# Kernel tuning notes

Measured on AMD Instinct MI355X. Metric: run time of the kernel, lower is better.

## Reference

```python
import jax, jax.numpy as jnp
import numpy as np

B, S, D, H, C = 128, 2048, 128, 128, 10  # batch, seq_len, input_size, hidden_size, num_classes


def setup_inputs() -> dict:
    key = jax.random.key(0)
    ks = jax.random.split(key, 11)
    k = 1.0 / np.sqrt(H)  # PyTorch RNN init scale
    u = lambda kk, shp: jax.random.uniform(kk, shp, jnp.float32, -k, k)
    return {
        "x": jax.random.normal(ks[0], (B, S, D), jnp.float32),
        # layer 0 (input D -> hidden H); gate order: r, z, n (PyTorch convention)
        "W_ih0": u(ks[1], (3 * H, D)), "W_hh0": u(ks[2], (3 * H, H)),
        "b_ih0": u(ks[3], (3 * H,)),   "b_hh0": u(ks[4], (3 * H,)),
        # layer 1 (hidden H -> hidden H)
        "W_ih1": u(ks[5], (3 * H, H)), "W_hh1": u(ks[6], (3 * H, H)),
        "b_ih1": u(ks[7], (3 * H,)),   "b_hh1": u(ks[8], (3 * H,)),
        # output linear H -> C
        "W_out": u(ks[9], (C, H)), "b_out": u(ks[10], (C,)),
    }


def _gru_layer(x, W_ih, W_hh, b_ih, b_hh):
    """Single unidirectional GRU layer, PyTorch math. x: [B,S,Din] -> ([B,S,H], h_last [B,H])."""
    Bs = x.shape[0]
    Hh = W_hh.shape[1]
    # Precompute all input projections in one big GEMM: [S,B,3H]
    xp = jnp.einsum('bsd,gd->sbg', x, W_ih) + b_ih
    h0 = jnp.zeros((Bs, Hh), x.dtype)

    def step(h, xp_t):
        hp = h @ W_hh.T + b_hh                      # [B,3H]
        xr, xz, xn = jnp.split(xp_t, 3, axis=-1)
        hr, hz, hn = jnp.split(hp, 3, axis=-1)
        r = jax.nn.sigmoid(xr + hr)                 # reset gate
        z = jax.nn.sigmoid(xz + hz)                 # update gate
        n = jnp.tanh(xn + r * hn)                   # new gate
        h_new = (1.0 - z) * n + z * h
        return h_new, h_new

    h_last, hs = jax.lax.scan(step, h0, xp)         # hs: [S,B,H]
    return jnp.transpose(hs, (1, 0, 2)), h_last


def reference(x, W_ih0, W_hh0, b_ih0, b_hh0, W_ih1, W_hh1, b_ih1, b_hh1, W_out, b_out):
    y0, _ = _gru_layer(x, W_ih0, W_hh0, b_ih0, b_hh0)
    _, h_last = _gru_layer(y0, W_ih1, W_hh1, b_ih1, b_hh1)
    # dropout between layers is disabled at inference (eval mode)
    return h_last @ W_out.T + b_out                 # [B,C] logits
```

## Files before the change

### kernel.cpp

```cpp
#include <hip/hip_runtime.h>
#include <hip/hip_bf16.h>


using bf16x8 = __attribute__((ext_vector_type(8))) short;
using s16x4  = __attribute__((ext_vector_type(4))) short;
using f32x4  = __attribute__((ext_vector_type(4))) float;
using f16x8  = __attribute__((ext_vector_type(8))) _Float16;
using f16x4  = __attribute__((ext_vector_type(4))) _Float16;
using u32x2  = __attribute__((ext_vector_type(2))) unsigned int;

#define S_LEN 2048
#define D_IN  128
#define HID   128
#define B_TOT 128
#define BC    16
#define PAD   136
#define G3    384
#define M_TOT (B_TOT * S_LEN)

#define CH    32
#define WIN   4
#define TILE_HALFS (BC * HID)
#define WGWIN_HALFS (WIN * CH * TILE_HALFS)

#define OP    104

__device__ __forceinline__ float bf2f(short s) {
  unsigned int u = ((unsigned int)(unsigned short)s) << 16;
  float f; __builtin_memcpy(&f, &u, 4); return f;
}
__device__ __forceinline__ short f2bf(float f) {
  unsigned int u; __builtin_memcpy(&u, &f, 4);
  u += 0x7fffu + ((u >> 16) & 1u);
  return (short)(u >> 16);
}
__device__ __forceinline__ float fast_sigmoid(float x) {
  return __builtin_amdgcn_rcpf(1.f + __expf(-x));
}
__device__ __forceinline__ float fast_tanh(float x) {
  return 2.f * __builtin_amdgcn_rcpf(1.f + __expf(-2.f * x)) - 1.f;
}
__device__ __forceinline__ f32x4 MFMA(bf16x8 a, bf16x8 b, f32x4 c) {
  return __builtin_amdgcn_mfma_f32_16x16x32_bf16(a, b, c, 0, 0, 0);
}
__device__ __forceinline__ f32x4 MFMA16(f16x8 a, f16x8 b, f32x4 c) {
  return __builtin_amdgcn_mfma_f32_16x16x32_f16(a, b, c, 0, 0, 0);
}
__device__ __forceinline__ void loadA(bf16x8 (&a)[4], const short* p) {
#pragma unroll
  for (int kq = 0; kq < 4; ++kq) a[kq] = *(const bf16x8*)(p + kq * 32);
}
__device__ __forceinline__ void loadA16(f16x8 (&a)[4], const _Float16* p) {
#pragma unroll
  for (int kq = 0; kq < 4; ++kq) a[kq] = *(const f16x8*)(p + kq * 32);
}
__device__ __forceinline__ void wg_barrier() {
  asm volatile("s_waitcnt lgkmcnt(0)\n\ts_barrier" ::: "memory");
}
__device__ __forceinline__ int ld_acq(const int* p) {
  return __hip_atomic_load(p, __ATOMIC_ACQUIRE, __HIP_MEMORY_SCOPE_AGENT);
}
__device__ __forceinline__ int ld_rlx(const int* p) {
  return __hip_atomic_load(p, __ATOMIC_RELAXED, __HIP_MEMORY_SCOPE_AGENT);
}
__device__ __forceinline__ void st_rel(int* p, int v) {
  __hip_atomic_store(p, v, __ATOMIC_RELEASE, __HIP_MEMORY_SCOPE_AGENT);
}

__global__ __launch_bounds__(256, 1) void xp0_gemm(
    const float* __restrict__ x, const float* __restrict__ Wih0,
    const float* __restrict__ bih0, const float* __restrict__ bhh0,
    _Float16* __restrict__ xp0)
{
  __shared__ _Float16 wlds[96 * PAD];
  __shared__ float bfold[G3];

  const int tid = threadIdx.x;
  const int w = tid >> 6, lane = tid & 63, nw = lane & 15, quad = lane >> 4;
  const int m0 = blockIdx.x * 64 + w * 16;

  for (int g = tid; g < G3; g += 256)
    bfold[g] = bih0[g] + (g < 256 ? bhh0[g] : 0.f);

  f16x8 af[4];
  const int arow = m0 + nw;
#pragma unroll
  for (int kq = 0; kq < 4; ++kq) {
    const float* p = x + (size_t)arow * D_IN + kq * 32 + quad * 8;
    float4 v0 = *(const float4*)p, v1 = *(const float4*)(p + 4);
    af[kq] = (f16x8){(_Float16)v0.x, (_Float16)v0.y, (_Float16)v0.z, (_Float16)v0.w,
                     (_Float16)v1.x, (_Float16)v1.y, (_Float16)v1.z, (_Float16)v1.w};
  }

  for (int grp = 0; grp < 4; ++grp) {
    __syncthreads();
    for (int i = tid; i < 96 * 128 / 4; i += 256) {
      const int idx = i * 4, row = idx >> 7, cc = idx & 127;
      float4 v = *(const float4*)(Wih0 + (size_t)(grp * 96 + row) * 128 + cc);
      f16x4 s = { (_Float16)v.x, (_Float16)v.y, (_Float16)v.z, (_Float16)v.w };
      *(f16x4*)&wlds[row * PAD + cc] = s;
    }
    __syncthreads();

    f32x4 acc[6];
#pragma unroll
    for (int i = 0; i < 6; ++i) acc[i] = (f32x4){0.f, 0.f, 0.f, 0.f};
#pragma unroll
    for (int tI = 0; tI < 6; ++tI)
#pragma unroll
      for (int kq = 0; kq < 4; ++kq) {
        f16x8 b = *(const f16x8*)&wlds[(tI * 16 + nw) * PAD + kq * 32 + quad * 8];
        acc[tI] = MFMA16(af[kq], b, acc[tI]);
      }

    __syncthreads();
#pragma unroll
    for (int tI = 0; tI < 6; ++tI) {
      const float bb = bfold[grp * 96 + tI * 16 + nw];
#pragma unroll
      for (int rr = 0; rr < 4; ++rr)
        wlds[(w * 16 + quad * 4 + rr) * OP + tI * 16 + nw] =
            (_Float16)(acc[tI][rr] + bb);
    }
    __syncthreads();
    {
      const int row = tid >> 2, ch = tid & 3;
      const _Float16* src = &wlds[row * OP + ch * 24];
      _Float16* dst = xp0 + (size_t)(blockIdx.x * 64 + row) * G3 + grp * 96 + ch * 24;
      *(f16x8*)(dst)      = *(const f16x8*)(src);
      *(f16x8*)(dst + 8)  = *(const f16x8*)(src + 8);
      *(f16x8*)(dst + 16) = *(const f16x8*)(src + 16);
    }
  }
}

__device__ __forceinline__ void mm3f(const f16x8 (&a)[4], const f16x8 (&W)[3][4],
                                     f32x4& r, f32x4& z, f32x4& n) {
#pragma unroll
  for (int kq = 0; kq < 4; ++kq) {
    r = MFMA16(a[kq], W[0][kq], r);
    z = MFMA16(a[kq], W[1][kq], z);
    n = MFMA16(a[kq], W[2][kq], n);
  }
}
__device__ __forceinline__ void mm3x2f(const f16x8 (&a)[4],
    const f16x8 (&Wa)[3][4], const f16x8 (&Wb)[3][4],
    f32x4& r1, f32x4& z1, f32x4& n1, f32x4& r2, f32x4& z2, f32x4& n2) {
#pragma unroll
  for (int kq = 0; kq < 4; ++kq) {
    r1 = MFMA16(a[kq], Wa[0][kq], r1);
    r2 = MFMA16(a[kq], Wb[0][kq], r2);
    z1 = MFMA16(a[kq], Wa[1][kq], z1);
    z2 = MFMA16(a[kq], Wb[1][kq], z2);
    n1 = MFMA16(a[kq], Wa[2][kq], n1);
    n2 = MFMA16(a[kq], Wb[2][kq], n2);
  }
}

__global__ __launch_bounds__(512, 2) void gru2_split(
    const _Float16* __restrict__ xp0,
    _Float16* __restrict__ win,
    int* __restrict__ ctrl,
    const float* __restrict__ Whh0, const float* __restrict__ bhh0,
    const float* __restrict__ Wih1, const float* __restrict__ Whh1,
    const float* __restrict__ bih1, const float* __restrict__ bhh1,
    const float* __restrict__ Wout, const float* __restrict__ bout,
    float* __restrict__ out)
{
  __shared__ _Float16 hf[2][BC * PAD];

  const int bid  = blockIdx.x;
  const int role = bid >> 3;
  const int g    = bid & 7;
  const int tid  = threadIdx.x;
  const int w    = tid >> 6;
  const int lane = tid & 63;
  const int nw   = lane & 15;
  const int quad = lane >> 4;
  const int col  = w * 16 + nw;
  const int b0   = g * BC;
  const int aoff = nw * PAD + quad * 8;

  int* flagp = ctrl + g;
  int* consp = ctrl + 8 + g;
  _Float16* win_g = win + (size_t)g * WGWIN_HALFS;

  for (int i = tid; i < 2 * BC * PAD; i += 512)
    ((_Float16*)hf)[i] = (_Float16)0.f;

  if (role == 0) {
    const float b0n_h = bhh0[256 + col];
    f16x8 Wh0[3][4];
#pragma unroll
    for (int gg = 0; gg < 3; ++gg)
#pragma unroll
      for (int kq = 0; kq < 4; ++kq) {
        const size_t o = (size_t)(gg * 128 + col) * HID + kq * 32 + quad * 8;
#pragma unroll
        for (int e = 0; e < 8; ++e) Wh0[gg][kq][e] = (_Float16)Whh0[o + e];
      }

    size_t xbase[4];
#pragma unroll
    for (int rr = 0; rr < 4; ++rr)
      xbase[rr] = (size_t)(b0 + quad * 4 + rr) * S_LEN * G3 + col;

    auto loadPK = [&](float (&P)[12], int t) {
      const size_t tG = (size_t)t * G3;
#pragma unroll
      for (int gg = 0; gg < 3; ++gg)
#pragma unroll
        for (int rr = 0; rr < 4; ++rr)
          P[gg * 4 + rr] = (float)xp0[xbase[rr] + tG + gg * 128];
    };

    float PA[12], PB[12];
    loadPK(PA, 0);
    loadPK(PB, 1);

    f32x4 h0r = {0.f, 0.f, 0.f, 0.f};
    const int cpo = (tid >> 5) * PAD + ((4 * tid) & 127);
    int cons_seen = 0;
    __syncthreads();

    auto pstep = [&](float (&P)[12], const int t, const int pr, const int pw) {
      if ((t & (CH - 1)) == 0) {
        const int need = (t >> 5) - (WIN - 1);
        if (need > 0 && cons_seen < need) {
          do { cons_seen = ld_rlx(consp);
               if (cons_seen < need) __builtin_amdgcn_s_sleep(8);
          } while (cons_seen < need);
        }
      }

      f32x4 ar = {P[0], P[1], P[2], P[3]};
      f32x4 az = {P[4], P[5], P[6], P[7]};
      f32x4 ahn = {b0n_h, b0n_h, b0n_h, b0n_h};
      f16x8 a[4];
      loadA16(a, &hf[pr][aoff]);
      mm3f(a, Wh0, ar, az, ahn);
#pragma unroll
      for (int rr = 0; rr < 4; ++rr) {
        float r = fast_sigmoid(ar[rr]);
        float z = fast_sigmoid(az[rr]);
        float n = fast_tanh(P[8 + rr] + r * ahn[rr]);
        float h = n + z * (h0r[rr] - n);
        h0r[rr] = h;
        hf[pw][(quad * 4 + rr) * PAD + col] = (_Float16)h;
      }
      wg_barrier();
      {
        u32x2 v;
        __builtin_memcpy(&v, &hf[pw][cpo], 8);
        _Float16* dst = win_g +
            ((size_t)((t >> 5) & (WIN - 1)) * CH + (t & (CH - 1))) * TILE_HALFS
            + 4 * tid;
        __builtin_nontemporal_store(v, (u32x2*)dst);
      }
      if ((t & (CH - 1)) == (CH - 1)) {
        __syncthreads();
        if (tid == 0) st_rel(flagp, (t >> 5) + 1);
      }
      const int tn = (t + 2 < S_LEN) ? t + 2 : t;
      loadPK(P, tn);
    };

#pragma unroll 1
    for (int tt = 0; tt < S_LEN; tt += 2) {
      pstep(PA, tt,     0, 1);
      pstep(PB, tt + 1, 1, 0);
    }
  } else {
    const float b1r   = bih1[col]       + bhh1[col];
    const float b1z   = bih1[128 + col] + bhh1[128 + col];
    const float b1n_i = bih1[256 + col];
    const float b1n_h = bhh1[256 + col];

    f16x8 Wi1[3][4], Wh1[3][4];
#pragma unroll
    for (int gg = 0; gg < 3; ++gg)
#pragma unroll
      for (int kq = 0; kq < 4; ++kq) {
        const size_t o = (size_t)(gg * 128 + col) * HID + kq * 32 + quad * 8;
#pragma unroll
        for (int e = 0; e < 8; ++e) {
          Wi1[gg][kq][e] = (_Float16)Wih1[o + e];
          Wh1[gg][kq][e] = (_Float16)Whh1[o + e];
        }
      }

    const int afroff = nw * 128 + quad * 8;
    f32x4 h1r = {0.f, 0.f, 0.f, 0.f};
    int seen = 0;
    __syncthreads();

    while (seen < 1) { seen = ld_acq(flagp);
                       if (seen < 1) __builtin_amdgcn_s_sleep(8); }
    f16x8 Anext[4];
    f32x4 xp1r = {b1r, b1r, b1r, b1r};
    f32x4 xp1z = {b1z, b1z, b1z, b1z};
    f32x4 xp1n = {b1n_i, b1n_i, b1n_i, b1n_i};
    {
      f16x8 A0[4];
#pragma unroll
      for (int kq = 0; kq < 4; ++kq)
        A0[kq] = *(const f16x8*)(win_g + afroff + kq * 32);
      mm3f(A0, Wi1, xp1r, xp1z, xp1n);
    }
#pragma unroll
    for (int kq = 0; kq < 4; ++kq)
      Anext[kq] = *(const f16x8*)(win_g + TILE_HALFS + afroff + kq * 32);

    auto cstep = [&](const int t, const int pr, const int pw) {
      if ((t & (CH - 1)) == 0 && tid == 0) st_rel(consp, t >> 5);
      f16x8 hfr[4];
      loadA16(hfr, &hf[pr][aoff]);
      f32x4 br  = xp1r;
      f32x4 bz  = xp1z;
      f32x4 bxn = xp1n;
      f32x4 bhn = {b1n_h, b1n_h, b1n_h, b1n_h};
      mm3f(hfr, Wh1, br, bz, bhn);
#pragma unroll
      for (int rr = 0; rr < 4; ++rr) {
        float r = fast_sigmoid(br[rr]);
        float z = fast_sigmoid(bz[rr]);
        float n = fast_tanh(bxn[rr] + r * bhn[rr]);
        float h = n + z * (h1r[rr] - n);
        h1r[rr] = h;
        hf[pw][(quad * 4 + rr) * PAD + col] = (_Float16)h;
      }
      xp1r = (f32x4){b1r, b1r, b1r, b1r};
      xp1z = (f32x4){b1z, b1z, b1z, b1z};
      xp1n = (f32x4){b1n_i, b1n_i, b1n_i, b1n_i};
      mm3f(Anext, Wi1, xp1r, xp1z, xp1n);
      const int tp2 = (t + 2 < S_LEN) ? t + 2 : S_LEN - 1;
      const int cn2 = (tp2 >> 5) + 1;
      if (seen < cn2) {
        do { seen = ld_acq(flagp);
             if (seen < cn2) __builtin_amdgcn_s_sleep(8);
        } while (seen < cn2);
      }
      {
        const _Float16* tp = win_g +
            ((size_t)((tp2 >> 5) & (WIN - 1)) * CH + (tp2 & (CH - 1))) * TILE_HALFS
            + afroff;
#pragma unroll
        for (int kq = 0; kq < 4; ++kq) Anext[kq] = *(const f16x8*)(tp + kq * 32);
      }
      wg_barrier();
    };

#pragma unroll 1
    for (int tt = 0; tt < S_LEN; tt += 2) {
      cstep(tt,     0, 1);
      cstep(tt + 1, 1, 0);
    }

    if (tid < BC * 10) {
      const int b = tid / 10, c = tid % 10;
      float s = bout[c];
      const _Float16* hh = &hf[0][b * PAD];
#pragma unroll 8
      for (int k = 0; k < HID; ++k)
        s += (float)hh[k] * Wout[c * HID + k];
      out[(size_t)(b0 + b) * 10 + c] = s;
    }
  }
}

__global__ __launch_bounds__(512, 2) void gru2_rec(
    const _Float16* __restrict__ xp0,
    const float* __restrict__ Whh0, const float* __restrict__ bhh0,
    const float* __restrict__ Wih1, const float* __restrict__ Whh1,
    const float* __restrict__ bih1, const float* __restrict__ bhh1,
    const float* __restrict__ Wout, const float* __restrict__ bout,
    float* __restrict__ out)
{
  __shared__ _Float16 h0f[2][BC * PAD];
  __shared__ _Float16 h1f[2][BC * PAD];

  const int tid  = threadIdx.x;
  const int w    = tid >> 6;
  const int lane = tid & 63;
  const int nw   = lane & 15;
  const int quad = lane >> 4;
  const int col  = w * 16 + nw;
  const int b0   = blockIdx.x * BC;

  for (int i = tid; i < 2 * BC * PAD; i += 512) {
    ((_Float16*)h0f)[i] = (_Float16)0.f;
    ((_Float16*)h1f)[i] = (_Float16)0.f;
  }

  const float b0n_h = bhh0[256 + col];
  const float b1r   = bih1[col]       + bhh1[col];
  const float b1z   = bih1[128 + col] + bhh1[128 + col];
  const float b1n_i = bih1[256 + col];
  const float b1n_h = bhh1[256 + col];

  f16x8 Wh0[3][4], Wi1[3][4], Wh1[3][4];
#pragma unroll
  for (int g = 0; g < 3; ++g) {
#pragma unroll
    for (int kq = 0; kq < 4; ++kq) {
      const size_t o = (size_t)(g * 128 + col) * HID + kq * 32 + quad * 8;
#pragma unroll
      for (int e = 0; e < 8; ++e) {
        Wh0[g][kq][e] = (_Float16)Whh0[o + e];
        Wi1[g][kq][e] = (_Float16)Wih1[o + e];
        Wh1[g][kq][e] = (_Float16)Whh1[o + e];
      }
    }
  }

  size_t xbase[4];
#pragma unroll
  for (int rr = 0; rr < 4; ++rr)
    xbase[rr] = (size_t)(b0 + quad * 4 + rr) * S_LEN * G3 + col;

  float P[12];
#pragma unroll
  for (int g = 0; g < 3; ++g)
#pragma unroll
    for (int rr = 0; rr < 4; ++rr)
      P[g * 4 + rr] = (float)xp0[xbase[rr] + g * 128];

  f32x4 h0r = {0.f, 0.f, 0.f, 0.f}, h1r = {0.f, 0.f, 0.f, 0.f};
  wg_barrier();

  const int aoff = nw * PAD + quad * 8;

  for (int t = 0; t < S_LEN; ++t) {
    const int pr = t & 1, pw = pr ^ 1;
    const int tn = (t + 1 < S_LEN) ? t + 1 : t;
    float Pn[12];
#pragma unroll
    for (int g = 0; g < 3; ++g)
#pragma unroll
      for (int rr = 0; rr < 4; ++rr)
        Pn[g * 4 + rr] = (float)xp0[xbase[rr] + (size_t)tn * G3 + g * 128];

    f32x4 ar  = {P[0], P[1], P[2], P[3]};
    f32x4 az  = {P[4], P[5], P[6], P[7]};
    f32x4 ahn = {b0n_h, b0n_h, b0n_h, b0n_h};
    f32x4 br  = {b1r, b1r, b1r, b1r};
    f32x4 bz  = {b1z, b1z, b1z, b1z};
    f32x4 bxn = {b1n_i, b1n_i, b1n_i, b1n_i};
    f32x4 bhn = {b1n_h, b1n_h, b1n_h, b1n_h};

    f16x8 a[4];
    loadA16(a, &h0f[pr][aoff]); mm3x2f(a, Wh0, Wi1, ar, az, ahn, br, bz, bxn);
    loadA16(a, &h1f[pr][aoff]); mm3f(a, Wh1, br, bz, bhn);

#pragma unroll
    for (int rr = 0; rr < 4; ++rr) {
      float r = fast_sigmoid(ar[rr]);
      float z = fast_sigmoid(az[rr]);
      float n = fast_tanh(P[8 + rr] + r * ahn[rr]);
      float h = n + z * (h0r[rr] - n);
      h0r[rr] = h;
      h0f[pw][(quad * 4 + rr) * PAD + col] = (_Float16)h;
    }
    if (t) {
#pragma unroll
      for (int rr = 0; rr < 4; ++rr) {
        float r = fast_sigmoid(br[rr]);
        float z = fast_sigmoid(bz[rr]);
        float n = fast_tanh(bxn[rr] + r * bhn[rr]);
        float h = n + z * (h1r[rr] - n);
        h1r[rr] = h;
        h1f[pw][(quad * 4 + rr) * PAD + col] = (_Float16)h;
      }
    }
#pragma unroll
    for (int i = 0; i < 12; ++i) P[i] = Pn[i];
    wg_barrier();
  }

  {
    f32x4 br  = {b1r, b1r, b1r, b1r};
    f32x4 bz  = {b1z, b1z, b1z, b1z};
    f32x4 bxn = {b1n_i, b1n_i, b1n_i, b1n_i};
    f32x4 bhn = {b1n_h, b1n_h, b1n_h, b1n_h};
    f16x8 a[4];
    loadA16(a, &h0f[0][aoff]); mm3f(a, Wi1, br, bz, bxn);
    loadA16(a, &h1f[0][aoff]); mm3f(a, Wh1, br, bz, bhn);
#pragma unroll
    for (int rr = 0; rr < 4; ++rr) {
      float r = fast_sigmoid(br[rr]);
      float z = fast_sigmoid(bz[rr]);
      float n = fast_tanh(bxn[rr] + r * bhn[rr]);
      float h = n + z * (h1r[rr] - n);
      h1f[1][(quad * 4 + rr) * PAD + col] = (_Float16)h;
    }
    wg_barrier();
  }

  if (tid < BC * 10) {
    const int b = tid / 10, c = tid % 10;
    float s = bout[c];
    const _Float16* hh = &h1f[1][b * PAD];
#pragma unroll 8
    for (int k = 0; k < HID; ++k)
      s += (float)hh[k] * Wout[c * HID + k];
    out[(size_t)(b0 + b) * 10 + c] = s;
  }
}

template<bool NSEP>
__device__ __forceinline__ void mm6(const bf16x8 (&a)[4], const bf16x8 (&W)[6][4],
                                    f32x4 (&acc)[6], f32x4 (&accn)[2]) {
#pragma unroll
  for (int tI = 0; tI < 6; ++tI)
#pragma unroll
    for (int kq = 0; kq < 4; ++kq) {
      if (NSEP && tI >= 4) accn[tI - 4] = MFMA(a[kq], W[tI][kq], accn[tI - 4]);
      else                 acc[tI]      = MFMA(a[kq], W[tI][kq], acc[tI]);
    }
}

__global__ __launch_bounds__(256, 1) void gru2_v1(
    const float* __restrict__ x,
    const float* __restrict__ Wih0, const float* __restrict__ Whh0,
    const float* __restrict__ bih0, const float* __restrict__ bhh0,
    const float* __restrict__ Wih1, const float* __restrict__ Whh1,
    const float* __restrict__ bih1, const float* __restrict__ bhh1,
    const float* __restrict__ Wout, const float* __restrict__ bout,
    float* __restrict__ out)
{
  __shared__ short h0hi[2][BC * PAD], h0lo[2][BC * PAD];
  __shared__ short h1hi[2][BC * PAD], h1lo[2][BC * PAD];
  __shared__ short xbhi[2][BC * PAD], xblo[2][BC * PAD];

  const int tid = threadIdx.x, w = tid >> 6, lane = tid & 63;
  const int nw = lane & 15, quad = lane >> 4, u0 = w * 32;
  const int b0 = blockIdx.x * BC;

  for (int i = tid; i < BC * PAD; i += 256) {
    h0hi[0][i] = 0; h0lo[0][i] = 0; h1hi[0][i] = 0; h1lo[0][i] = 0;
  }
  const size_t xelem = (size_t)(b0 + (tid >> 4)) * (size_t)(S_LEN * D_IN) + (size_t)((tid & 15) * 8);
  const int xsoff = (tid >> 4) * PAD + (tid & 15) * 8;

  auto load_x = [&](int t, bf16x8& xhi, bf16x8& xlo) {
    const size_t o = xelem + (size_t)t * D_IN;
    float4 v0 = *(const float4*)(x + o), v1 = *(const float4*)(x + o + 4);
    float v[8] = {v0.x, v0.y, v0.z, v0.w, v1.x, v1.y, v1.z, v1.w};
#pragma unroll
    for (int e = 0; e < 8; ++e) {
      short h = f2bf(v[e]); xhi[e] = h; xlo[e] = f2bf(v[e] - bf2f(h));
    }
  };
  { bf16x8 xh, xl; load_x(0, xh, xl);
    *(bf16x8*)&xbhi[0][xsoff] = xh; *(bf16x8*)&xblo[0][xsoff] = xl; }

  float brz0[4], bn0[4], brz1[4], bn1[4];
#pragma unroll
  for (int i = 0; i < 2; ++i) {
    const int c = u0 + i * 16 + nw;
    brz0[i] = bih0[c] + bhh0[c];     brz0[2 + i] = bih0[128 + c] + bhh0[128 + c];
    bn0[i] = bih0[256 + c];          bn0[2 + i] = bhh0[256 + c];
    brz1[i] = bih1[c] + bhh1[c];     brz1[2 + i] = bih1[128 + c] + bhh1[128 + c];
    bn1[i] = bih1[256 + c];          bn1[2 + i] = bhh1[256 + c];
  }

  bf16x8 W0[6][4], Wh0f[6][4], W1[6][4], Wh1f[6][4];
#pragma unroll
  for (int tI = 0; tI < 6; ++tI) {
    const int rb = (tI >> 1) * 128 + u0 + (tI & 1) * 16 + nw;
#pragma unroll
    for (int kq = 0; kq < 4; ++kq) {
      const size_t o = (size_t)rb * HID + kq * 32 + quad * 8;
#pragma unroll
      for (int e = 0; e < 8; ++e) {
        W0[tI][kq][e] = f2bf(Wih0[o + e]);  Wh0f[tI][kq][e] = f2bf(Whh0[o + e]);
        W1[tI][kq][e] = f2bf(Wih1[o + e]);  Wh1f[tI][kq][e] = f2bf(Whh1[o + e]);
      }
    }
  }

  f32x4 h0reg[2] = {{0,0,0,0},{0,0,0,0}}, h1reg[2] = {{0,0,0,0},{0,0,0,0}};
  const f32x4 ZV = {0.f, 0.f, 0.f, 0.f};
  __syncthreads();
  const int aoff = nw * PAD + quad * 8;

  auto gates = [&](const f32x4 (&acc)[6], const f32x4 (&accn)[2], f32x4 (&hreg)[2],
                   const float (&brz)[4], const float (&bn)[4],
                   short* dhi, short* dlo) {
#pragma unroll
    for (int i = 0; i < 2; ++i) {
      const int c = u0 + i * 16 + nw;
#pragma unroll
      for (int rr = 0; rr < 4; ++rr) {
        float rv = fast_sigmoid(acc[i][rr] + brz[i]);
        float zv = fast_sigmoid(acc[2 + i][rr] + brz[2 + i]);
        float nv = fast_tanh((acc[4 + i][rr] + bn[i]) + rv * (accn[i][rr] + bn[2 + i]));
        float h = (1.f - zv) * nv + zv * hreg[i][rr];
        hreg[i][rr] = h;
        short hi = f2bf(h);
        const int row = quad * 4 + rr;
        dhi[row * PAD + c] = hi;
        dlo[row * PAD + c] = f2bf(h - bf2f(hi));
      }
    }
  };

  for (int t = 0; t < S_LEN; ++t) {
    const int pr = t & 1, pw = pr ^ 1;
    const int t1 = (t + 1 < S_LEN) ? t + 1 : t;
    bf16x8 xh, xl; load_x(t1, xh, xl);

    f32x4 acc[6], accn[2];
#pragma unroll
    for (int i = 0; i < 6; ++i) acc[i] = ZV;
#pragma unroll
    for (int i = 0; i < 2; ++i) accn[i] = ZV;
    bf16x8 a[4];
    loadA(a, &xbhi[pr][aoff]); mm6<false>(a, W0, acc, accn);
    loadA(a, &xblo[pr][aoff]); mm6<false>(a, W0, acc, accn);
    loadA(a, &h0hi[pr][aoff]); mm6<true >(a, Wh0f, acc, accn);
    loadA(a, &h0lo[pr][aoff]); mm6<true >(a, Wh0f, acc, accn);
    gates(acc, accn, h0reg, brz0, bn0, h0hi[pw], h0lo[pw]);
    __syncthreads();

#pragma unroll
    for (int i = 0; i < 6; ++i) acc[i] = ZV;
#pragma unroll
    for (int i = 0; i < 2; ++i) accn[i] = ZV;
    loadA(a, &h0hi[pw][aoff]); mm6<false>(a, W1, acc, accn);
    loadA(a, &h0lo[pw][aoff]); mm6<false>(a, W1, acc, accn);
    loadA(a, &h1hi[pr][aoff]); mm6<true >(a, Wh1f, acc, accn);
    loadA(a, &h1lo[pr][aoff]); mm6<true >(a, Wh1f, acc, accn);
    *(bf16x8*)&xbhi[pw][xsoff] = xh;
    *(bf16x8*)&xblo[pw][xsoff] = xl;
    gates(acc, accn, h1reg, brz1, bn1, h1hi[pw], h1lo[pw]);
    __syncthreads();
  }

  if (tid < BC * 10) {
    const int b = tid / 10, c = tid % 10;
    float s = bout[c];
    const short* hh = &h1hi[0][b * PAD];
    const short* hl = &h1lo[0][b * PAD];
#pragma unroll 8
    for (int k = 0; k < HID; ++k)
      s += (bf2f(hh[k]) + bf2f(hl[k])) * Wout[c * HID + k];
    out[(size_t)(b0 + b) * 10 + c] = s;
  }
}

extern "C" void kernel_launch(void* const* d_in, const int* in_sizes, int n_in,
                              void* d_out, int out_size, void* d_ws, size_t ws_size,
                              hipStream_t stream) {
  (void)in_sizes; (void)n_in; (void)out_size;
  const float* x    = (const float*)d_in[0];
  const float* Wih0 = (const float*)d_in[1];
  const float* Whh0 = (const float*)d_in[2];
  const float* bih0 = (const float*)d_in[3];
  const float* bhh0 = (const float*)d_in[4];
  const float* Wih1 = (const float*)d_in[5];
  const float* Whh1 = (const float*)d_in[6];
  const float* bih1 = (const float*)d_in[7];
  const float* bhh1 = (const float*)d_in[8];
  const float* Wout = (const float*)d_in[9];
  const float* bout = (const float*)d_in[10];
  float* out = (float*)d_out;

  const size_t XPB  = (size_t)M_TOT * G3 * sizeof(_Float16);
  const size_t WINB = 8ull * WGWIN_HALFS * sizeof(_Float16);
  const size_t REQ  = XPB + WINB + 64;

  if (ws_size >= REQ) {
    char* ws = (char*)d_ws;
    _Float16* xp0  = (_Float16*)ws;
    _Float16* wing = (_Float16*)(ws + XPB);
    int*      ctrl = (int*)(ws + XPB + WINB);
    (void)hipMemsetAsync(ctrl, 0, 64, stream);
    xp0_gemm<<<dim3(M_TOT / 64), dim3(256), 0, stream>>>(
        x, Wih0, bih0, bhh0, xp0);
    gru2_split<<<dim3(16), dim3(512), 0, stream>>>(
        xp0, wing, ctrl, Whh0, bhh0, Wih1, Whh1, bih1, bhh1, Wout, bout, out);
  } else if (ws_size >= XPB) {
    xp0_gemm<<<dim3(M_TOT / 64), dim3(256), 0, stream>>>(
        x, Wih0, bih0, bhh0, (_Float16*)d_ws);
    gru2_rec<<<dim3(B_TOT / BC), dim3(512), 0, stream>>>(
        (const _Float16*)d_ws, Whh0, bhh0, Wih1, Whh1, bih1, bhh1, Wout, bout, out);
  } else {
    gru2_v1<<<dim3(B_TOT / BC), dim3(256), 0, stream>>>(
        x, Wih0, Whh0, bih0, bhh0, Wih1, Whh1, bih1, bhh1, Wout, bout, out);
  }
}
```

Before: 2.305 ms.

## Fuse input-projection GEMM into recurrent kernel with per-chunk readiness flags

```diff
diff --git a/kernel.cpp b/kernel.cpp
--- a/kernel.cpp
+++ b/kernel.cpp
@@ -24,6 +24,8 @@
 #define WGWIN_HALFS (WIN * CH * TILE_HALFS)
 
 #define OP    104
+#define P1B   2048
+#define TCH   128
 
 __device__ __forceinline__ float bf2f(short s) {
   unsigned int u = ((unsigned int)(unsigned short)s) << 16;
@@ -67,116 +69,101 @@
   __hip_atomic_store(p, v, __ATOMIC_RELEASE, __HIP_MEMORY_SCOPE_AGENT);
 }
 
-__global__ __launch_bounds__(256, 1) void xp0_gemm(
+__global__ __launch_bounds__(512, 2) void gru2_all(
     const float* __restrict__ x, const float* __restrict__ Wih0,
     const float* __restrict__ bih0, const float* __restrict__ bhh0,
-    _Float16* __restrict__ xp0)
-{
-  __shared__ _Float16 wlds[96 * PAD];
-  __shared__ float bfold[G3];
-
-  const int tid = threadIdx.x;
-  const int w = tid >> 6, lane = tid & 63, nw = lane & 15, quad = lane >> 4;
-  const int m0 = blockIdx.x * 64 + w * 16;
-
-  for (int g = tid; g < G3; g += 256)
-    bfold[g] = bih0[g] + (g < 256 ? bhh0[g] : 0.f);
-
-  f16x8 af[4];
-  const int arow = m0 + nw;
-#pragma unroll
-  for (int kq = 0; kq < 4; ++kq) {
-    const float* p = x + (size_t)arow * D_IN + kq * 32 + quad * 8;
-    float4 v0 = *(const float4*)p, v1 = *(const float4*)(p + 4);
-    af[kq] = (f16x8){(_Float16)v0.x, (_Float16)v0.y, (_Float16)v0.z, (_Float16)v0.w,
-                     (_Float16)v1.x, (_Float16)v1.y, (_Float16)v1.z, (_Float16)v1.w};
-  }
-
-  for (int grp = 0; grp < 4; ++grp) {
-    __syncthreads();
-    for (int i = tid; i < 96 * 128 / 4; i += 256) {
-      const int idx = i * 4, row = idx >> 7, cc = idx & 127;
-      float4 v = *(const float4*)(Wih0 + (size_t)(grp * 96 + row) * 128 + cc);
-      f16x4 s = { (_Float16)v.x, (_Float16)v.y, (_Float16)v.z, (_Float16)v.w };
-      *(f16x4*)&wlds[row * PAD + cc] = s;
-    }
-    __syncthreads();
-
-    f32x4 acc[6];
-#pragma unroll
-    for (int i = 0; i < 6; ++i) acc[i] = (f32x4){0.f, 0.f, 0.f, 0.f};
-#pragma unroll
-    for (int tI = 0; tI < 6; ++tI)
-#pragma unroll
-      for (int kq = 0; kq < 4; ++kq) {
-        f16x8 b = *(const f16x8*)&wlds[(tI * 16 + nw) * PAD + kq * 32 + quad * 8];
-        acc[tI] = MFMA16(af[kq], b, acc[tI]);
-      }
-
-    __syncthreads();
-#pragma unroll
-    for (int tI = 0; tI < 6; ++tI) {
-      const float bb = bfold[grp * 96 + tI * 16 + nw];
-#pragma unroll
-      for (int rr = 0; rr < 4; ++rr)
-        wlds[(w * 16 + quad * 4 + rr) * OP + tI * 16 + nw] =
-            (_Float16)(acc[tI][rr] + bb);
-    }
-    __syncthreads();
-    {
-      const int row = tid >> 2, ch = tid & 3;
-      const _Float16* src = &wlds[row * OP + ch * 24];
-      _Float16* dst = xp0 + (size_t)(blockIdx.x * 64 + row) * G3 + grp * 96 + ch * 24;
-      *(f16x8*)(dst)      = *(const f16x8*)(src);
-      *(f16x8*)(dst + 8)  = *(const f16x8*)(src + 8);
-      *(f16x8*)(dst + 16) = *(const f16x8*)(src + 16);
-    }
-  }
-}
-
-__device__ __forceinline__ void mm3f(const f16x8 (&a)[4], const f16x8 (&W)[3][4],
-                                     f32x4& r, f32x4& z, f32x4& n) {
-#pragma unroll
-  for (int kq = 0; kq < 4; ++kq) {
-    r = MFMA16(a[kq], W[0][kq], r);
-    z = MFMA16(a[kq], W[1][kq], z);
-    n = MFMA16(a[kq], W[2][kq], n);
-  }
-}
-__device__ __forceinline__ void mm3x2f(const f16x8 (&a)[4],
-    const f16x8 (&Wa)[3][4], const f16x8 (&Wb)[3][4],
-    f32x4& r1, f32x4& z1, f32x4& n1, f32x4& r2, f32x4& z2, f32x4& n2) {
-#pragma unroll
-  for (int kq = 0; kq < 4; ++kq) {
-    r1 = MFMA16(a[kq], Wa[0][kq], r1);
-    r2 = MFMA16(a[kq], Wb[0][kq], r2);
-    z1 = MFMA16(a[kq], Wa[1][kq], z1);
-    z2 = MFMA16(a[kq], Wb[1][kq], z2);
-    n1 = MFMA16(a[kq], Wa[2][kq], n1);
-    n2 = MFMA16(a[kq], Wb[2][kq], n2);
-  }
-}
-
-__global__ __launch_bounds__(512, 2) void gru2_split(
-    const _Float16* __restrict__ xp0,
-    _Float16* __restrict__ win,
-    int* __restrict__ ctrl,
-    const float* __restrict__ Whh0, const float* __restrict__ bhh0,
+    _Float16* __restrict__ xp0,
+    _Float16* __restrict__ win, int* __restrict__ ctrl,
+    const float* __restrict__ Whh0, const float* __restrict__ bhh0b,
     const float* __restrict__ Wih1, const float* __restrict__ Whh1,
     const float* __restrict__ bih1, const float* __restrict__ bhh1,
     const float* __restrict__ Wout, const float* __restrict__ bout,
     float* __restrict__ out)
 {
-  __shared__ _Float16 hf[2][BC * PAD];
+  __shared__ __align__(16) char smem[28160];
 
   const int bid  = blockIdx.x;
-  const int role = bid >> 3;
-  const int g    = bid & 7;
   const int tid  = threadIdx.x;
   const int w    = tid >> 6;
   const int lane = tid & 63;
   const int nw   = lane & 15;
   const int quad = lane >> 4;
+
+  if (bid >= 16) {
+    _Float16* wlds = (_Float16*)smem;
+    float* bfold = (float*)(smem + 26624);
+
+    const int p  = bid - 16;
+    const int b  = p & 127;
+    const int tc = p >> 7;
+    const int mb = b * S_LEN + tc * TCH;
+    const int m0 = mb + w * 16;
+
+    for (int g = tid; g < G3; g += 512)
+      bfold[g] = bih0[g] + (g < 256 ? bhh0[g] : 0.f);
+
+    f16x8 af[4];
+    const int arow = m0 + nw;
+#pragma unroll
+    for (int kq = 0; kq < 4; ++kq) {
+      const float* px = x + (size_t)arow * D_IN + kq * 32 + quad * 8;
+      float4 v0 = *(const float4*)px, v1 = *(const float4*)(px + 4);
+      af[kq] = (f16x8){(_Float16)v0.x, (_Float16)v0.y, (_Float16)v0.z, (_Float16)v0.w,
+                       (_Float16)v1.x, (_Float16)v1.y, (_Float16)v1.z, (_Float16)v1.w};
+    }
+
+    for (int grp = 0; grp < 4; ++grp) {
+      __syncthreads();
+      for (int i = tid; i < 96 * 128 / 4; i += 512) {
+        const int idx = i * 4, row = idx >> 7, cc = idx & 127;
+        float4 v = *(const float4*)(Wih0 + (size_t)(grp * 96 + row) * 128 + cc);
+        f16x4 s = { (_Float16)v.x, (_Float16)v.y, (_Float16)v.z, (_Float16)v.w };
+        *(f16x4*)&wlds[row * PAD + cc] = s;
+      }
+      __syncthreads();
+
+      f32x4 acc[6];
+#pragma unroll
+      for (int i = 0; i < 6; ++i) acc[i] = (f32x4){0.f, 0.f, 0.f, 0.f};
+#pragma unroll
+      for (int tI = 0; tI < 6; ++tI)
+#pragma unroll
+        for (int kq = 0; kq < 4; ++kq) {
+          f16x8 bfr = *(const f16x8*)&wlds[(tI * 16 + nw) * PAD + kq * 32 + quad * 8];
+          acc[tI] = MFMA16(af[kq], bfr, acc[tI]);
+        }
+
+      __syncthreads();
+#pragma unroll
+      for (int tI = 0; tI < 6; ++tI) {
+        const float bb = bfold[grp * 96 + tI * 16 + nw];
+#pragma unroll
+        for (int rr = 0; rr < 4; ++rr)
+          wlds[(w * 16 + quad * 4 + rr) * OP + tI * 16 + nw] =
+              (_Float16)(acc[tI][rr] + bb);
+      }
+      __syncthreads();
+      {
+        const int row = tid >> 2, ch = tid & 3;
+        const _Float16* src = &wlds[row * OP + ch * 24];
+        _Float16* dst = xp0 + (size_t)(mb + row) * G3 + grp * 96 + ch * 24;
+        *(f16x8*)(dst)      = *(const f16x8*)(src);
+        *(f16x8*)(dst + 8)  = *(const f16x8*)(src + 8);
+        *(f16x8*)(dst + 16) = *(const f16x8*)(src + 16);
+      }
+    }
+    __syncthreads();
+    if (tid == 0)
+      (void)__hip_atomic_fetch_add(ctrl + 16 + tc, 1, __ATOMIC_RELEASE,
+                                   __HIP_MEMORY_SCOPE_AGENT);
+    return;
+  }
+
+  _Float16 (&hf)[2][BC * PAD] =
+      *reinterpret_cast<_Float16 (*)[2][BC * PAD]>(smem);
+
+  const int role = bid >> 3;
+  const int g    = bid & 7;
   const int col  = w * 16 + nw;
   const int b0   = g * BC;
   const int aoff = nw * PAD + quad * 8;
@@ -189,7 +176,7 @@
     ((_Float16*)hf)[i] = (_Float16)0.f;
 
   if (role == 0) {
-    const float b0n_h = bhh0[256 + col];
+    const float b0n_h = bhh0b[256 + col];
     f16x8 Wh0[3][4];
 #pragma unroll
     for (int gg = 0; gg < 3; ++gg)
@@ -204,6 +191,13 @@
 #pragma unroll
     for (int rr = 0; rr < 4; ++rr)
       xbase[rr] = (size_t)(b0 + quad * 4 + rr) * S_LEN * G3 + col;
+
+    int chunk_seen = 0;
+    auto wait_chunk = [&](int c) {
+      if (chunk_seen > c) return;
+      while (ld_acq(ctrl + 16 + c) < 128) __builtin_amdgcn_s_sleep(8);
+      chunk_seen = c + 1;
+    };
 
     auto loadPK = [&](float (&P)[12], int t) {
       const size_t tG = (size_t)t * G3;
@@ -215,6 +209,7 @@
     };
 
     float PA[12], PB[12];
+    wait_chunk(0);
     loadPK(PA, 0);
     loadPK(PB, 1);
 
@@ -238,7 +233,13 @@
       f32x4 ahn = {b0n_h, b0n_h, b0n_h, b0n_h};
       f16x8 a[4];
       loadA16(a, &hf[pr][aoff]);
-      mm3f(a, Wh0, ar, az, ahn);
+      mm3f_inline: ;
+#pragma unroll
+      for (int kq = 0; kq < 4; ++kq) {
+        ar  = MFMA16(a[kq], Wh0[0][kq], ar);
+        az  = MFMA16(a[kq], Wh0[1][kq], az);
+        ahn = MFMA16(a[kq], Wh0[2][kq], ahn);
+      }
 #pragma unroll
       for (int rr = 0; rr < 4; ++rr) {
         float r = fast_sigmoid(ar[rr]);
@@ -262,6 +263,8 @@
         if (tid == 0) st_rel(flagp, (t >> 5) + 1);
       }
       const int tn = (t + 2 < S_LEN) ? t + 2 : t;
+      const int tc2 = tn >> 7;
+      if (tc2 != (t >> 7)) wait_chunk(tc2);
       loadPK(P, tn);
     };
 
@@ -305,7 +308,12 @@
 #pragma unroll
       for (int kq = 0; kq < 4; ++kq)
         A0[kq] = *(const f16x8*)(win_g + afroff + kq * 32);
-      mm3f(A0, Wi1, xp1r, xp1z, xp1n);
+#pragma unroll
+      for (int kq = 0; kq < 4; ++kq) {
+        xp1r = MFMA16(A0[kq], Wi1[0][kq], xp1r);
+        xp1z = MFMA16(A0[kq], Wi1[1][kq], xp1z);
+        xp1n = MFMA16(A0[kq], Wi1[2][kq], xp1n);
+      }
     }
 #pragma unroll
     for (int kq = 0; kq < 4; ++kq)
@@ -319,7 +327,12 @@
       f32x4 bz  = xp1z;
       f32x4 bxn = xp1n;
       f32x4 bhn = {b1n_h, b1n_h, b1n_h, b1n_h};
-      mm3f(hfr, Wh1, br, bz, bhn);
+#pragma unroll
+      for (int kq = 0; kq < 4; ++kq) {
+        br  = MFMA16(hfr[kq], Wh1[0][kq], br);
+        bz  = MFMA16(hfr[kq], Wh1[1][kq], bz);
+        bhn = MFMA16(hfr[kq], Wh1[2][kq], bhn);
+      }
 #pragma unroll
       for (int rr = 0; rr < 4; ++rr) {
         float r = fast_sigmoid(br[rr]);
@@ -332,7 +345,12 @@
       xp1r = (f32x4){b1r, b1r, b1r, b1r};
       xp1z = (f32x4){b1z, b1z, b1z, b1z};
       xp1n = (f32x4){b1n_i, b1n_i, b1n_i, b1n_i};
-      mm3f(Anext, Wi1, xp1r, xp1z, xp1n);
+#pragma unroll
+      for (int kq = 0; kq < 4; ++kq) {
+        xp1r = MFMA16(Anext[kq], Wi1[0][kq], xp1r);
+        xp1z = MFMA16(Anext[kq], Wi1[1][kq], xp1z);
+        xp1n = MFMA16(Anext[kq], Wi1[2][kq], xp1n);
+      }
       const int tp2 = (t + 2 < S_LEN) ? t + 2 : S_LEN - 1;
       const int cn2 = (tp2 >> 5) + 1;
       if (seen < cn2) {
@@ -365,6 +383,88 @@
         s += (float)hh[k] * Wout[c * HID + k];
       out[(size_t)(b0 + b) * 10 + c] = s;
     }
+  }
+}
+
+__global__ __launch_bounds__(256, 1) void xp0_gemm(
+    const float* __restrict__ x, const float* __restrict__ Wih0,
+    const float* __restrict__ bih0, const float* __restrict__ bhh0,
+    _Float16* __restrict__ xp0)
+{
+  __shared__ _Float16 wlds[96 * PAD];
+  __shared__ float bfold[G3];
+
+  const int tid = threadIdx.x;
+  const int w = tid >> 6, lane = tid & 63, nw = lane & 15, quad = lane >> 4;
+  const int m0 = blockIdx.x * 64 + w * 16;
+
+  for (int g = tid; g < G3; g += 256)
+    bfold[g] = bih0[g] + (g < 256 ? bhh0[g] : 0.f);
+
+  f16x8 af[4];
+  const int arow = m0 + nw;
+#pragma unroll
+  for (int kq = 0; kq < 4; ++kq) {
+    const float* p = x + (size_t)arow * D_IN + kq * 32 + quad * 8;
+    float4 v0 = *(const float4*)p, v1 = *(const float4*)(p + 4);
+    af[kq] = (f16x8){(_Float16)v0.x, (_Float16)v0.y, (_Float16)v0.z, (_Float16)v0.w,
+                     (_Float16)v1.x, (_Float16)v1.y, (_Float16)v1.z, (_Float16)v1.w};
+  }
+
+  for (int grp = 0; grp < 4; ++grp) {
+    __syncthreads();
+    for (int i = tid; i < 96 * 128 / 4; i += 256) {
+      const int idx = i * 4, row = idx >> 7, cc = idx & 127;
+      float4 v = *(const float4*)(Wih0 + (size_t)(grp * 96 + row) * 128 + cc);
+      f16x4 s = { (_Float16)v.x, (_Float16)v.y, (_Float16)v.z, (_Float16)v.w };
+      *(f16x4*)&wlds[row * PAD + cc] = s;
+    }
+    __syncthreads();
+
+    f32x4 acc[6];
+#pragma unroll
+    for (int i = 0; i < 6; ++i) acc[i] = (f32x4){0.f, 0.f, 0.f, 0.f};
+#pragma unroll
+    for (int tI = 0; tI < 6; ++tI)
+#pragma unroll
+      for (int kq = 0; kq < 4; ++kq) {
+        f16x8 b = *(const f16x8*)&wlds[(tI * 16 + nw) * PAD + kq * 32 + quad * 8];
+        acc[tI] = MFMA16(af[kq], b, acc[tI]);
+      }
+
+#pragma unroll
+    for (int tI = 0; tI < 6; ++tI) {
+      const int g = grp * 96 + tI * 16 + nw;
+      const float bb = bfold[g];
+#pragma unroll
+      for (int rr = 0; rr < 4; ++rr) {
+        const int m = m0 + quad * 4 + rr;
+        xp0[(size_t)m * G3 + g] = (_Float16)(acc[tI][rr] + bb);
+      }
+    }
+  }
+}
+
+__device__ __forceinline__ void mm3f(const f16x8 (&a)[4], const f16x8 (&W)[3][4],
+                                     f32x4& r, f32x4& z, f32x4& n) {
+#pragma unroll
+  for (int kq = 0; kq < 4; ++kq) {
+    r = MFMA16(a[kq], W[0][kq], r);
+    z = MFMA16(a[kq], W[1][kq], z);
+    n = MFMA16(a[kq], W[2][kq], n);
+  }
+}
+__device__ __forceinline__ void mm3x2f(const f16x8 (&a)[4],
+    const f16x8 (&Wa)[3][4], const f16x8 (&Wb)[3][4],
+    f32x4& r1, f32x4& z1, f32x4& n1, f32x4& r2, f32x4& z2, f32x4& n2) {
+#pragma unroll
+  for (int kq = 0; kq < 4; ++kq) {
+    r1 = MFMA16(a[kq], Wa[0][kq], r1);
+    r2 = MFMA16(a[kq], Wb[0][kq], r2);
+    z1 = MFMA16(a[kq], Wa[1][kq], z1);
+    z2 = MFMA16(a[kq], Wb[1][kq], z2);
+    n1 = MFMA16(a[kq], Wa[2][kq], n1);
+    n2 = MFMA16(a[kq], Wb[2][kq], n2);
   }
 }
 
@@ -668,18 +768,17 @@
 
   const size_t XPB  = (size_t)M_TOT * G3 * sizeof(_Float16);
   const size_t WINB = 8ull * WGWIN_HALFS * sizeof(_Float16);
-  const size_t REQ  = XPB + WINB + 64;
+  const size_t REQ  = XPB + WINB + 128;
 
   if (ws_size >= REQ) {
     char* ws = (char*)d_ws;
     _Float16* xp0  = (_Float16*)ws;
     _Float16* wing = (_Float16*)(ws + XPB);
     int*      ctrl = (int*)(ws + XPB + WINB);
-    (void)hipMemsetAsync(ctrl, 0, 64, stream);
-    xp0_gemm<<<dim3(M_TOT / 64), dim3(256), 0, stream>>>(
-        x, Wih0, bih0, bhh0, xp0);
-    gru2_split<<<dim3(16), dim3(512), 0, stream>>>(
-        xp0, wing, ctrl, Whh0, bhh0, Wih1, Whh1, bih1, bhh1, Wout, bout, out);
+    (void)hipMemsetAsync(ctrl, 0, 128, stream);
+    gru2_all<<<dim3(16 + P1B), dim3(512), 0, stream>>>(
+        x, Wih0, bih0, bhh0, xp0, wing, ctrl,
+        Whh0, bhh0, Wih1, Whh1, bih1, bhh1, Wout, bout, out);
   } else if (ws_size >= XPB) {
     xp0_gemm<<<dim3(M_TOT / 64), dim3(256), 0, stream>>>(
         x, Wih0, bih0, bhh0, (_Float16*)d_ws);
```

After: 2.348 ms. Within noise of the previous version (+1.9%).
